# Performance work log

Measured on AMD Instinct MI355X. Metric: run time of the kernel, lower is better.

## Reference

```python
import jax, jax.numpy as jnp
import numpy as np
import math

B, NX, NY = 2, 2048, 2048
CX, CY = 1024, 1024
KEY_CH, VAL_CH, HEADS = 1024, 1024, 16


def setup_inputs() -> dict:
    key = jax.random.key(0)
    ks = jax.random.split(key, 10)
    s = lambda fan_in: 1.0 / math.sqrt(fan_in)
    inp = {
        "x": jax.random.normal(ks[0], (B, NX, CX), dtype=jnp.float32),
        "y": jax.random.normal(ks[1], (B, NY, CY), dtype=jnp.float32),
        "Wq": jax.random.uniform(ks[2], (CX, KEY_CH), jnp.float32, -s(CX), s(CX)),
        "bq": jax.random.uniform(ks[3], (KEY_CH,), jnp.float32, -s(CX), s(CX)),
        "Wk": jax.random.uniform(ks[4], (CY, KEY_CH), jnp.float32, -s(CY), s(CY)),
        "bk": jax.random.uniform(ks[5], (KEY_CH,), jnp.float32, -s(CY), s(CY)),
        "Wv": jax.random.uniform(ks[6], (CY, VAL_CH), jnp.float32, -s(CY), s(CY)),
        "bv": jax.random.uniform(ks[7], (VAL_CH,), jnp.float32, -s(CY), s(CY)),
        "Wo": jax.random.uniform(ks[8], (VAL_CH, CX), jnp.float32, -s(VAL_CH), s(VAL_CH)),
        "bo": jax.random.uniform(ks[9], (CX,), jnp.float32, -s(VAL_CH), s(VAL_CH)),
    }
    return inp


def reference(x, y, Wq, bq, Wk, bk, Wv, bv, Wo, bo):
    Bx, Nx, _ = x.shape
    By, Ny, _ = y.shape
    dk = KEY_CH // HEADS
    dv = VAL_CH // HEADS
    # projections
    q = (x @ Wq + bq).reshape(Bx, Nx, HEADS, dk)  # contiguous head slices == reshape
    k = (y @ Wk + bk).reshape(By, Ny, HEADS, dk)
    v = (y @ Wv + bv).reshape(By, Ny, HEADS, dv)
    # NOTE: original scales by 1/sqrt(Ny) (sequence length), not 1/sqrt(dk)
    scores = jnp.einsum("bnhd,bmhd->bhnm", q, k) / jnp.sqrt(jnp.float32(Ny))
    attn = jax.nn.softmax(scores, axis=-1)
    out = jnp.einsum("bhnm,bmhd->bnhd", attn, v).reshape(Bx, Nx, VAL_CH)
    out = jax.nn.relu(out @ Wo + bo)
    # dropout(p=0.2) is identity in eval mode
    return out
```

## Files before the change

### kernel.cpp

```cpp
#include <hip/hip_runtime.h>
#include <hip/hip_bf16.h>

typedef __bf16 bf16;
typedef __attribute__((ext_vector_type(8))) __bf16 bf16x8;
typedef __attribute__((ext_vector_type(4))) __bf16 bf16x4;
typedef __attribute__((ext_vector_type(4))) float f32x4;
typedef __attribute__((ext_vector_type(16))) float f32x16;
typedef __attribute__((ext_vector_type(4))) unsigned int u32x4;
typedef __attribute__((ext_vector_type(2))) unsigned int u32x2;

__device__ __forceinline__ void gload_lds16(const void* g, void* l) {
  __builtin_amdgcn_global_load_lds((const __attribute__((address_space(1))) void*)g,
                                   (__attribute__((address_space(3))) void*)l, 16, 0, 0);
}

__device__ __forceinline__ float exp2_b(float x) { return __builtin_amdgcn_exp2f(x); }
__device__ __forceinline__ void plswap_b(unsigned& a, unsigned& b) {
  u32x2 r = __builtin_amdgcn_permlane32_swap(a, b, false, false);
  a = r[0]; b = r[1];
}
__device__ __forceinline__ unsigned cvtpk(float lo, float hi) {
  unsigned r;
  asm("v_cvt_pk_bf16_f32 %0, %1, %2" : "=v"(r) : "v"(lo), "v"(hi));
  return r;
}

__global__ __launch_bounds__(256) void cvtw_kernel(
    const float* __restrict__ x, const float* __restrict__ y,
    bf16* __restrict__ xb, bf16* __restrict__ yb,
    const float* __restrict__ W0, const float* __restrict__ W1,
    const float* __restrict__ W2, const float* __restrict__ W3,
    bf16* __restrict__ T0, bf16* __restrict__ T1,
    bf16* __restrict__ T2, bf16* __restrict__ T3) {
  __shared__ float t[32][33];
  const int bid = blockIdx.x, tid = threadIdx.x;
  if (bid < 4096) {
    const int z = bid >> 10, rem = bid & 1023;
    const int bx = rem & 31, by = rem >> 5;
    const float* W; bf16* T;
    switch (z) {
      case 0: W = W0; T = T0; break;
      case 1: W = W1; T = T1; break;
      case 2: W = W2; T = T2; break;
      default: W = W3; T = T3; break;
    }
    const int tx = tid & 31, ty = tid >> 5;
    const int bn = bx * 32, bk = by * 32;
#pragma unroll
    for (int i = 0; i < 32; i += 8)
      t[ty + i][tx] = W[(size_t)(bk + ty + i) * 1024 + bn + tx];
    __syncthreads();
#pragma unroll
    for (int i = 0; i < 32; i += 8)
      T[(size_t)(bn + ty + i) * 1024 + bk + tx] = (bf16)t[tx][ty + i];
  } else {
    const int n4 = 1048576;
    int i = (bid - 4096) * 256 + tid;
    const float4* in = (const float4*)x; bf16x4* out = (bf16x4*)xb;
    if (i >= n4) { in = (const float4*)y; out = (bf16x4*)yb; i -= n4; }
    float4 v = in[i];
    bf16x4 o;
    o[0] = (bf16)v.x; o[1] = (bf16)v.y; o[2] = (bf16)v.z; o[3] = (bf16)v.w;
    out[i] = o;
  }
}

__global__ __launch_bounds__(512, 6) void gemm_qkv(
    const bf16* __restrict__ xb, const bf16* __restrict__ yb,
    const bf16* __restrict__ Wqt, const bf16* __restrict__ Wkt, const bf16* __restrict__ Wvt,
    const float* __restrict__ bq, const float* __restrict__ bk, const float* __restrict__ bv,
    bf16* __restrict__ Qb, bf16* __restrict__ Kb, bf16* __restrict__ Vtb) {
  constexpr int K = 1024;
  constexpr float QSCALE = (float)(1.4426950408889634 / 45.254833995939045);
  __shared__ bf16 As[2][128 * 32];
  __shared__ bf16 Bs[2][128 * 32];
  const int z = blockIdx.z;
  const bf16* A  = (z == 0) ? xb : yb;
  const bf16* Bt = (z == 0) ? Wqt : (z == 1) ? Wkt : Wvt;
  const float* bias = (z == 0) ? bq : (z == 1) ? bk : bv;

  const int tid = threadIdx.x;
  const int wave = tid >> 6, lane = tid & 63;
  const int g = lane >> 4, r15 = lane & 15;
  const int m0 = blockIdx.x * 128, n0 = blockIdx.y * 128;
  const int wr = wave >> 2, wc = wave & 3;

  f32x4 acc[4][2] = {};

  const int rowA = tid >> 2, chA = tid & 3;

  auto stage = [&](int buf, int k0) {
    gload_lds16(A  + (size_t)(m0 + rowA) * K + k0 + chA * 8, (char*)As[buf] + tid * 16);
    gload_lds16(Bt + (size_t)(n0 + rowA) * K + k0 + chA * 8, (char*)Bs[buf] + tid * 16);
  };

  stage(0, 0);
  __syncthreads();
  int cur = 0;
  for (int t = 0; t < K / 32; ++t) {
    if (t + 1 < K / 32) stage(cur ^ 1, (t + 1) * 32);
    bf16x8 af[4], bfr[2];
#pragma unroll
    for (int mi = 0; mi < 4; ++mi)
      af[mi] = *(const bf16x8*)((const char*)As[cur] + ((wr * 64 + mi * 16 + r15) * 64 + g * 16));
#pragma unroll
    for (int nj = 0; nj < 2; ++nj)
      bfr[nj] = *(const bf16x8*)((const char*)Bs[cur] + ((wc * 32 + nj * 16 + r15) * 64 + g * 16));
#pragma unroll
    for (int mi = 0; mi < 4; ++mi)
#pragma unroll
      for (int nj = 0; nj < 2; ++nj)
        acc[mi][nj] = __builtin_amdgcn_mfma_f32_16x16x32_bf16(af[mi], bfr[nj], acc[mi][nj], 0, 0, 0);
    __syncthreads();
    cur ^= 1;
  }

  const float scl = (z == 0) ? QSCALE : 1.0f;
#pragma unroll
  for (int mi = 0; mi < 4; ++mi) {
#pragma unroll
    for (int nj = 0; nj < 2; ++nj) {
      int row = m0 + wr * 64 + mi * 16 + g * 4;
      int col = n0 + wc * 32 + nj * 16 + r15;
      float bv_ = bias[col];
      if (z < 2) {
        bf16* C = (z == 0) ? Qb : Kb;
#pragma unroll
        for (int r = 0; r < 4; ++r)
          C[(size_t)(row + r) * 1024 + col] = (bf16)((acc[mi][nj][r] + bv_) * scl);
      } else {
        int b = row >> 11, n = row & 2047;
        bf16x4 pkv;
#pragma unroll
        for (int r = 0; r < 4; ++r)
          pkv[r] = (bf16)(acc[mi][nj][r] + bv_);
        *(bf16x4*)(Vtb + ((size_t)b * 1024 + col) * 2048 + n) = pkv;
      }
    }
  }
}

__global__ __launch_bounds__(512, 4) void gemm_out(
    const bf16* __restrict__ A, const bf16* __restrict__ Bt,
    const float* __restrict__ bias, float* __restrict__ C) {
  constexpr int K = 1024;
  __shared__ bf16 As[2][128 * 32];
  __shared__ bf16 Bs[2][64 * 32];
  const int tid = threadIdx.x;
  const int wave = tid >> 6, lane = tid & 63;
  const int g = lane >> 4, r15 = lane & 15;
  const int m0 = blockIdx.x * 128, n0 = blockIdx.y * 64;
  const int wr = wave >> 1, wc = wave & 1;

  f32x4 acc[2][2] = {};

  const int rowA = tid >> 2, chA = tid & 3;

  auto stage = [&](int buf, int k0) {
    gload_lds16(A + (size_t)(m0 + rowA) * K + k0 + chA * 8, (char*)As[buf] + tid * 16);
    if (tid < 256)
      gload_lds16(Bt + (size_t)(n0 + rowA) * K + k0 + chA * 8, (char*)Bs[buf] + tid * 16);
  };

  stage(0, 0);
  __syncthreads();
  int cur = 0;
  for (int t = 0; t < K / 32; ++t) {
    if (t + 1 < K / 32) stage(cur ^ 1, (t + 1) * 32);
    bf16x8 af[2], bfr[2];
#pragma unroll
    for (int mi = 0; mi < 2; ++mi)
      af[mi] = *(const bf16x8*)((const char*)As[cur] + ((wr * 32 + mi * 16 + r15) * 64 + g * 16));
#pragma unroll
    for (int nj = 0; nj < 2; ++nj)
      bfr[nj] = *(const bf16x8*)((const char*)Bs[cur] + ((wc * 32 + nj * 16 + r15) * 64 + g * 16));
#pragma unroll
    for (int mi = 0; mi < 2; ++mi)
#pragma unroll
      for (int nj = 0; nj < 2; ++nj)
        acc[mi][nj] = __builtin_amdgcn_mfma_f32_16x16x32_bf16(af[mi], bfr[nj], acc[mi][nj], 0, 0, 0);
    __syncthreads();
    cur ^= 1;
  }

#pragma unroll
  for (int mi = 0; mi < 2; ++mi)
#pragma unroll
    for (int nj = 0; nj < 2; ++nj) {
      int row = m0 + wr * 32 + mi * 16 + g * 4;
      int col = n0 + wc * 32 + nj * 16 + r15;
      float bv_ = bias[col];
#pragma unroll
      for (int r = 0; r < 4; ++r)
        C[(size_t)(row + r) * 1024 + col] = fmaxf(acc[mi][nj][r] + bv_, 0.0f);
    }
}

__global__ __launch_bounds__(256, 4) void attn_kernel(
    const bf16* __restrict__ Q, const bf16* __restrict__ Kin,
    const bf16* __restrict__ Vt, bf16* __restrict__ Oa) {
  __shared__ bf16 Ks[2][64 * 64];
  __shared__ bf16 Vs[2][64 * 64];
  const int tid = threadIdx.x;
  const int w = tid >> 6, lane = tid & 63;
  const int q5 = lane & 31, h = lane >> 5;
  const int kh = w & 1, qh = w >> 1;

  int i = blockIdx.y * 32 + blockIdx.x;
  int xcd = i & 7, slot = i >> 3;
  int bh = xcd * 4 + (slot >> 5), qt = slot & 31;
  int b = bh >> 4, hd = bh & 15;

  const bf16* Qg = Q + ((size_t)b * 2048 + qt * 64 + qh * 32) * 1024 + hd * 64;
  const bf16* Kg = Kin + (size_t)b * 2048 * 1024 + hd * 64;
  const bf16* Vg = Vt + ((size_t)b * 1024 + hd * 64) * 2048;

  bf16x8 qf[4];
#pragma unroll
  for (int ks = 0; ks < 4; ++ks)
    qf[ks] = *(const bf16x8*)(Qg + (size_t)q5 * 1024 + ks * 16 + h * 8);

  f32x16 o[2] = {};
  float ls = 0.0f;

  auto stage = [&](int buf, int kv0) {
#pragma unroll
    for (int ii = 0; ii < 2; ++ii) {
      int c = tid + ii * 256;
      int row = c >> 3;
      int sl = (c & 7) ^ (row & 7) ^ ((row >> 3) & 1);
      gload_lds16(Kg + (size_t)(kv0 + row) * 1024 + sl * 8, (char*)Ks[buf] + c * 16);
      gload_lds16(Vg + (size_t)row * 2048 + kv0 + sl * 8, (char*)Vs[buf] + c * 16);
    }
  };

  stage(0, 0);
  __syncthreads();
  int cur = 0;

  const int krow = kh * 32 + q5;
  const int kswz = (krow & 7) ^ ((krow >> 3) & 1);

  unsigned uA[8], uB[8];
  bf16x8 vA[4], vB[4];

  auto phase = [&](int t, unsigned (&uin)[8], unsigned (&uout)[8],
                   bf16x8 (&vin)[4], bf16x8 (&vout)[4], bool doStage, bool doPV) {
    if (doStage) stage(cur ^ 1, (t + 1) * 64);

    f32x16 s = {};
    __builtin_amdgcn_s_setprio(1);
#pragma unroll
    for (int ks = 0; ks < 4; ++ks) {
      bf16x8 kf = *(const bf16x8*)((const char*)Ks[cur] + krow * 128 + (((2 * ks + h) ^ kswz) << 4));
      s = __builtin_amdgcn_mfma_f32_32x32x16_bf16(kf, qf[ks], s, 0, 0, 0);
    }

#pragma unroll
    for (int j = 0; j < 2; ++j) {
      const int db = kh ^ j;
      const int vrow0 = db * 32 + q5;
      const int vswz = (vrow0 & 7) ^ ((vrow0 >> 3) & 1);
#pragma unroll
      for (int kap = 0; kap < 2; ++kap)
        vout[2 * j + kap] = *(const bf16x8*)((const char*)Vs[cur] + vrow0 * 128 +
                                             (((4 * kh + 2 * kap + h) ^ vswz) << 4));
    }

    if (doPV) {
#pragma unroll
      for (int j = 0; j < 2; ++j)
#pragma unroll
        for (int kap = 0; kap < 2; ++kap) {
          u32x4 uw;
          uw[0] = uin[4 * kap + 0]; uw[1] = uin[4 * kap + 1];
          uw[2] = uin[4 * kap + 2]; uw[3] = uin[4 * kap + 3];
          bf16x8 pa = __builtin_bit_cast(bf16x8, uw);
          o[j] = __builtin_amdgcn_mfma_f32_32x32x16_bf16(pa, vin[2 * j + kap], o[j], 0, 0, 0);
        }
    }
    __builtin_amdgcn_s_setprio(0);

    float e[16];
#pragma unroll
    for (int jj = 0; jj < 16; ++jj) e[jj] = exp2_b(s[jj]);
    ls += ((((e[0] + e[1]) + (e[2] + e[3])) + ((e[4] + e[5]) + (e[6] + e[7]))) +
           (((e[8] + e[9]) + (e[10] + e[11])) + ((e[12] + e[13]) + (e[14] + e[15]))));
#pragma unroll
    for (int p = 0; p < 8; ++p) uout[p] = cvtpk(e[2 * p], e[2 * p + 1]);
    plswap_b(uout[0], uout[2]); plswap_b(uout[1], uout[3]);
    plswap_b(uout[4], uout[6]); plswap_b(uout[5], uout[7]);

    __syncthreads();
    cur ^= 1;
  };

  phase(0, uB, uA, vB, vA, true, false);
  for (int t = 1; t < 31; t += 2) {
    phase(t, uA, uB, vA, vB, true, true);
    phase(t + 1, uB, uA, vB, vA, true, true);
  }
  phase(31, uA, uB, vA, vB, false, true);
#pragma unroll
  for (int j = 0; j < 2; ++j)
#pragma unroll
    for (int kap = 0; kap < 2; ++kap) {
      u32x4 uw;
      uw[0] = uB[4 * kap + 0]; uw[1] = uB[4 * kap + 1];
      uw[2] = uB[4 * kap + 2]; uw[3] = uB[4 * kap + 3];
      bf16x8 pa = __builtin_bit_cast(bf16x8, uw);
      o[j] = __builtin_amdgcn_mfma_f32_32x32x16_bf16(pa, vB[2 * j + kap], o[j], 0, 0, 0);
    }

  ls += __shfl_xor(ls, 32);

  float* osh = (float*)Ks;
  float* lsf = (float*)Vs;
  *(f32x16*)(osh + ((size_t)(w * 64 + lane)) * 16) = o[1];
  if (h == 0) lsf[w * 32 + q5] = ls;
  __syncthreads();

  const int pw = w ^ 1;
  float lt = ls + lsf[pw * 32 + q5];
  float iv = __builtin_amdgcn_rcpf(lt);
  f32x16 p = *(const f32x16*)(osh + ((size_t)(pw * 64 + lane)) * 16);
#pragma unroll
  for (int g4 = 0; g4 < 4; ++g4)
#pragma unroll
    for (int r = 0; r < 4; ++r) {
      int qr = g4 * 8 + 4 * h + r;
      float il = __shfl(iv, qr);
      size_t row = (size_t)b * 2048 + qt * 64 + qh * 32 + qr;
      Oa[row * 1024 + hd * 64 + kh * 32 + q5] = (bf16)((o[0][g4 * 4 + r] + p[g4 * 4 + r]) * il);
    }
}

extern "C" void kernel_launch(void* const* d_in, const int* in_sizes, int n_in,
                              void* d_out, int out_size, void* d_ws, size_t ws_size,
                              hipStream_t stream) {
  (void)in_sizes; (void)n_in; (void)out_size; (void)ws_size;
  const float* x  = (const float*)d_in[0];
  const float* y  = (const float*)d_in[1];
  const float* Wq = (const float*)d_in[2];
  const float* bq = (const float*)d_in[3];
  const float* Wk = (const float*)d_in[4];
  const float* bk = (const float*)d_in[5];
  const float* Wv = (const float*)d_in[6];
  const float* bv = (const float*)d_in[7];
  const float* Wo = (const float*)d_in[8];
  const float* bo = (const float*)d_in[9];

  char* ws = (char*)d_ws;
  bf16* xb  = (bf16*)(ws + 0);
  bf16* yb  = (bf16*)(ws + 8388608);
  bf16* Qb  = (bf16*)(ws + 16777216);
  bf16* Kb  = (bf16*)(ws + 25165824);
  bf16* Vtb = (bf16*)(ws + 33554432);
  bf16* Oab = (bf16*)(ws + 41943040);
  bf16* Wqt = (bf16*)(ws + 50331648);
  bf16* Wkt = (bf16*)(ws + 52428800);
  bf16* Wvt = (bf16*)(ws + 54525952);
  bf16* Wot = (bf16*)(ws + 56623104);

  cvtw_kernel<<<12288, 256, 0, stream>>>(x, y, xb, yb, Wq, Wk, Wv, Wo, Wqt, Wkt, Wvt, Wot);
  gemm_qkv<<<dim3(32, 8, 3), 512, 0, stream>>>(xb, yb, Wqt, Wkt, Wvt, bq, bk, bv, Qb, Kb, Vtb);
  attn_kernel<<<dim3(32, 32), dim3(256), 0, stream>>>(Qb, Kb, Vtb, Oab);
  gemm_out<<<dim3(32, 16), 512, 0, stream>>>(Oab, Wot, bo, (float*)d_out);
}
```

Before: 118.4 us.

## Triple-buffer K/V tiles in attention kernel with partial vmcnt waits

Moves the attention kernel's K/V shared-memory staging from double to triple buffering, prefetching two tiles ahead. The full __syncthreads is replaced by an explicit s_waitcnt vmcnt(4) plus s_barrier, so the next tile's loads can stay in flight across iterations. This aims to hide global-load latency better, at the cost of more LDS per block (48KB) and the occupancy hint dropping from 4 to 3 blocks per CU.

```diff
diff --git a/kernel.cpp b/kernel.cpp
--- a/kernel.cpp
+++ b/kernel.cpp
@@ -196,11 +196,11 @@
     }
 }
 
-__global__ __launch_bounds__(256, 4) void attn_kernel(
+__global__ __launch_bounds__(256, 3) void attn_kernel(
     const bf16* __restrict__ Q, const bf16* __restrict__ Kin,
     const bf16* __restrict__ Vt, bf16* __restrict__ Oa) {
-  __shared__ bf16 Ks[2][64 * 64];
-  __shared__ bf16 Vs[2][64 * 64];
+  __shared__ bf16 Ks[3][64 * 64];
+  __shared__ bf16 Vs[3][64 * 64];
   const int tid = threadIdx.x;
   const int w = tid >> 6, lane = tid & 63;
   const int q5 = lane & 31, h = lane >> 5;
@@ -235,8 +235,10 @@
   };
 
   stage(0, 0);
-  __syncthreads();
-  int cur = 0;
+  stage(1, 64);
+  asm volatile("s_waitcnt vmcnt(4)" ::: "memory");
+  __builtin_amdgcn_s_barrier();
+  __builtin_amdgcn_sched_barrier(0);
 
   const int krow = kh * 32 + q5;
   const int kswz = (krow & 7) ^ ((krow >> 3) & 1);
@@ -245,14 +247,16 @@
   bf16x8 vA[4], vB[4];
 
   auto phase = [&](int t, unsigned (&uin)[8], unsigned (&uout)[8],
-                   bf16x8 (&vin)[4], bf16x8 (&vout)[4], bool doStage, bool doPV) {
-    if (doStage) stage(cur ^ 1, (t + 1) * 64);
+                   bf16x8 (&vin)[4], bf16x8 (&vout)[4], bool doPV) {
+    int rb = t % 3;
+    const bool doStage = (t + 2 <= 31);
+    if (doStage) stage((t + 2) % 3, (t + 2) * 64);
 
     f32x16 s = {};
     __builtin_amdgcn_s_setprio(1);
 #pragma unroll
     for (int ks = 0; ks < 4; ++ks) {
-      bf16x8 kf = *(const bf16x8*)((const char*)Ks[cur] + krow * 128 + (((2 * ks + h) ^ kswz) << 4));
+      bf16x8 kf = *(const bf16x8*)((const char*)Ks[rb] + krow * 128 + (((2 * ks + h) ^ kswz) << 4));
       s = __builtin_amdgcn_mfma_f32_32x32x16_bf16(kf, qf[ks], s, 0, 0, 0);
     }
 
@@ -263,7 +267,7 @@
       const int vswz = (vrow0 & 7) ^ ((vrow0 >> 3) & 1);
 #pragma unroll
       for (int kap = 0; kap < 2; ++kap)
-        vout[2 * j + kap] = *(const bf16x8*)((const char*)Vs[cur] + vrow0 * 128 +
+        vout[2 * j + kap] = *(const bf16x8*)((const char*)Vs[rb] + vrow0 * 128 +
                                              (((4 * kh + 2 * kap + h) ^ vswz) << 4));
     }
 
@@ -291,16 +295,21 @@
     plswap_b(uout[0], uout[2]); plswap_b(uout[1], uout[3]);
     plswap_b(uout[4], uout[6]); plswap_b(uout[5], uout[7]);
 
-    __syncthreads();
-    cur ^= 1;
+    if (doStage) {
+      asm volatile("s_waitcnt vmcnt(4) lgkmcnt(0)" ::: "memory");
+    } else {
+      asm volatile("s_waitcnt vmcnt(0) lgkmcnt(0)" ::: "memory");
+    }
+    __builtin_amdgcn_s_barrier();
+    __builtin_amdgcn_sched_barrier(0);
   };
 
-  phase(0, uB, uA, vB, vA, true, false);
+  phase(0, uB, uA, vB, vA, false);
   for (int t = 1; t < 31; t += 2) {
-    phase(t, uA, uB, vA, vB, true, true);
-    phase(t + 1, uB, uA, vB, vA, true, true);
-  }
-  phase(31, uA, uB, vA, vB, false, true);
+    phase(t, uA, uB, vA, vB, true);
+    phase(t + 1, uB, uA, vB, vA, true);
+  }
+  phase(31, uA, uB, vA, vB, true);
 #pragma unroll
   for (int j = 0; j < 2; ++j)
 #pragma unroll
```

Result: slower. 129.8 us (+9.6%).
